# Performance work log

Measured on AMD Instinct MI355X. Metric: run time of the kernel, lower is better.

The kernel has to match this reference:

```python
import jax, jax.numpy as jnp
import numpy as np
import itertools

# hyperparameters (match init_kwargs cfg)
V_SIZE = 32000; D = 768; H = 12; NL = 2
K_BITS = 4; L_TAB = 4; M_COPIES = 2; HID = 3072
DK = D // H; R = 1 << K_BITS; EPS = 1e-6; RMS_EPS = 1e-5

def _protos_T():
    # corners of the {-1,+1}^K hypercube, transposed -> [K, R]
    corners = np.array(list(itertools.product([-1.0, 1.0], repeat=K_BITS)), dtype=np.float32)
    return jnp.asarray(corners.T)

def setup_inputs() -> dict:
    key = jax.random.key(0)
    ks = jax.random.split(key, 14)
    s = 0.02
    return {
        "in_idx": jax.random.randint(ks[0], (1, 1024), 0, V_SIZE),
        "tok_emb": jax.random.normal(ks[1], (V_SIZE, D), jnp.float32) * s,
        "norm1_w": jnp.ones((NL, D), jnp.float32),
        "qw": jax.random.normal(ks[2], (NL, D, D), jnp.float32) * s,
        "kw": jax.random.normal(ks[3], (NL, D, D), jnp.float32) * s,
        "vw": jax.random.normal(ks[4], (NL, D, D), jnp.float32) * s,
        "ow": jax.random.normal(ks[5], (NL, D, D), jnp.float32) * s,
        "ob": jnp.zeros((NL, D), jnp.float32),
        "norm2_w": jnp.ones((NL, D), jnp.float32),
        "ff_w1": jax.random.normal(ks[6], (NL, D, HID), jnp.float32) * s,
        "ff_w2": jax.random.normal(ks[7], (NL, D, HID), jnp.float32) * s,
        "ff_w3": jax.random.normal(ks[8], (NL, HID, D), jnp.float32) * s,
        "final_norm_w": jnp.ones((D,), jnp.float32),
        "out_w": jax.random.normal(ks[9], (D, V_SIZE), jnp.float32) * s,
        "planes_T": jax.random.normal(ks[10], (NL, M_COPIES, DK, L_TAB * K_BITS), jnp.float32),
    }

def _rmsnorm(x, w):
    return x * jax.lax.rsqrt(jnp.mean(x * x, axis=-1, keepdims=True) + RMS_EPS) * w

def _race_attention(h, qw, kw, vw, ow, ob, planes, protos_T):
    B, T, _ = h.shape
    Q = (h @ qw).reshape(B, T, H, DK)
    Kt = (h @ kw).reshape(B, T, H, DK)
    Vt = (h @ vw).reshape(B, T, H, DK)
    # RoPE (split-even/odd, concat halves variant, start position 0)
    theta = 10000.0 ** (-jnp.arange(0, DK, 2, dtype=jnp.float32) / DK)
    freq = jnp.arange(T, dtype=jnp.float32)[:, None] * theta[None, :]  # [T, DK/2]
    sin = jnp.sin(freq)[None, :, None, :]
    cos = jnp.cos(freq)[None, :, None, :]
    def rope(z):
        e, o = z[..., ::2], z[..., 1::2]
        return jnp.concatenate([e * cos - o * sin, e * sin + o * cos], axis=-1)
    Q, Kt = rope(Q), rope(Kt)
    to_hb = lambda z: jnp.transpose(z, (0, 2, 1, 3)).reshape(B * H, T, DK)
    Qh, Kh, Vh = to_hb(Q), to_hb(Kt), to_hb(Vt)
    N = M_COPIES * B * H
    scale = jnp.sqrt(jnp.float32(DK))
    # random-plane projections per model copy m: [M, BH, T, L*K]
    projK = jnp.einsum('ntd,mds->mnts', Kh, planes).reshape(N, T, L_TAB, K_BITS)
    projQ = jnp.einsum('ntd,mds->mnts', Qh, planes).reshape(N, T, L_TAB, K_BITS)
    probsK = jax.nn.softmax((jnp.tanh(projK) / scale) @ protos_T, axis=-1)  # [N,T,L,R]
    probsQ = jax.nn.softmax((jnp.tanh(projQ) / scale) @ protos_T, axis=-1)
    Vn = jnp.broadcast_to(Vh[None], (M_COPIES, B * H, T, DK)).reshape(N, T, DK)
    # causal prefix sums over time
    A_pref = jnp.cumsum(probsK, axis=1)                                     # [N,T,L,R]
    B_pref = jnp.cumsum(probsK[..., None] * Vn[:, :, None, None, :], axis=1)  # [N,T,L,R,DK]
    E_pref = B_pref / (A_pref[..., None] + EPS)
    out2 = jnp.einsum('ntlr,ntlrd->ntd', probsQ, E_pref)                    # [N,T,DK]
    out_h = out2.reshape(M_COPIES, B, H, T, DK).transpose(0, 1, 3, 2, 4)    # [M,B,T,H,DK]
    m = out_h.mean(axis=0)                                                  # [B,T,H,DK]
    # faithful to the source: permute to [B,H,T,DK] then row-major reshape to [B,T,H*DK]
    out = jnp.transpose(m, (0, 2, 1, 3)).reshape(B, T, H * DK)
    return out @ ow + ob

def reference(in_idx, tok_emb, norm1_w, qw, kw, vw, ow, ob, norm2_w,
              ff_w1, ff_w2, ff_w3, final_norm_w, out_w, planes_T):
    protos_T = _protos_T()
    x = tok_emb[in_idx]  # [B,T,D]
    for l in range(NL):
        h = _rmsnorm(x, norm1_w[l])
        x = x + _race_attention(h, qw[l], kw[l], vw[l], ow[l], ob[l], planes_T[l], protos_T)
        h = _rmsnorm(x, norm2_w[l])
        x = x + (jax.nn.silu(h @ ff_w1[l]) * (h @ ff_w2[l])) @ ff_w3[l]
    x = _rmsnorm(x, final_norm_w)
    return x @ out_w  # logits [B,T,V]
```

## Files before the change

kernel.cpp:

```cpp
#include <hip/hip_runtime.h>
#include <hip/hip_bf16.h>

#define T_SEQ 1024
#define D_MODEL 768
#define QKVW 2304
#define NHEAD 12
#define NLAYER 2
#define MCOPY 2
#define HID_DIM 3072
#define VSIZE 32000
#define NCH 32
#define TL 32

typedef __attribute__((ext_vector_type(8))) short short8;
typedef __attribute__((ext_vector_type(4))) float f32x4;

__device__ __forceinline__ short f2bf(float f) {
  unsigned u = __builtin_bit_cast(unsigned, f);
  u = (u + 0x7FFFu + ((u >> 16) & 1u)) >> 16;
  return (short)u;
}

__global__ __launch_bounds__(64) void stc_k(float* __restrict__ stc) {
  int t = blockIdx.x;
  int i = threadIdx.x;
  if (i < 32) {
    float theta = powf(10000.0f, -(float)i / 32.0f);
    float s, c;
    sincosf((float)t * theta, &s, &c);
    stc[t * 64 + 2 * i] = c;
    stc[t * 64 + 2 * i + 1] = s;
  }
}

__global__ __launch_bounds__(256) void embed_norm_k(const int* __restrict__ idx,
                                                    const float* __restrict__ emb,
                                                    const float* __restrict__ w,
                                                    float* __restrict__ x,
                                                    short* __restrict__ out) {
  int t = blockIdx.x, tid = threadIdx.x;
  int r = idx[t];
  float v[3];
  float ss = 0.f;
  #pragma unroll
  for (int j = 0; j < 3; ++j) {
    int i = tid + j * 256;
    float val = emb[(size_t)r * D_MODEL + i];
    x[(size_t)t * D_MODEL + i] = val;
    v[j] = val;
    ss += val * val;
  }
  __shared__ float red[256];
  red[tid] = ss; __syncthreads();
  for (int s = 128; s > 0; s >>= 1) {
    if (tid < s) red[tid] += red[tid + s];
    __syncthreads();
  }
  float inv = rsqrtf(red[0] / (float)D_MODEL + 1e-5f);
  #pragma unroll
  for (int j = 0; j < 3; ++j) {
    int i = tid + j * 256;
    out[(size_t)t * D_MODEL + i] = f2bf(v[j] * inv * w[i]);
  }
}

__global__ __launch_bounds__(256) void add_norm_k(float* __restrict__ x,
                                                  const float* __restrict__ parts,
                                                  int nparts,
                                                  const float* __restrict__ bias,
                                                  const float* __restrict__ w,
                                                  short* __restrict__ out) {
  int t = blockIdx.x, tid = threadIdx.x;
  float v[3];
  float ss = 0.f;
  #pragma unroll
  for (int j = 0; j < 3; ++j) {
    int i = tid + j * 256;
    float val = x[(size_t)t * D_MODEL + i];
    if (bias) val += bias[i];
    for (int p = 0; p < nparts; ++p)
      val += parts[(size_t)p * (T_SEQ * D_MODEL) + (size_t)t * D_MODEL + i];
    v[j] = val;
    ss += val * val;
  }
  __shared__ float red[256];
  red[tid] = ss; __syncthreads();
  for (int s = 128; s > 0; s >>= 1) {
    if (tid < s) red[tid] += red[tid + s];
    __syncthreads();
  }
  float inv = rsqrtf(red[0] / (float)D_MODEL + 1e-5f);
  #pragma unroll
  for (int j = 0; j < 3; ++j) {
    int i = tid + j * 256;
    if (nparts || bias) x[(size_t)t * D_MODEL + i] = v[j];
    out[(size_t)t * D_MODEL + i] = f2bf(v[j] * inv * w[i]);
  }
}

__device__ __forceinline__ void tr_tile(const float* __restrict__ W,
                                        short* __restrict__ WT, int K, int N,
                                        int n0, int k0, int tx, int ty) {
  __shared__ float tile[32][33];
  #pragma unroll
  for (int i = 0; i < 4; ++i)
    tile[ty + 8 * i][tx] = W[(size_t)(k0 + ty + 8 * i) * N + n0 + tx];
  __syncthreads();
  #pragma unroll
  for (int i = 0; i < 4; ++i)
    WT[(size_t)(n0 + ty + 8 * i) * K + k0 + tx] = f2bf(tile[tx][ty + 8 * i]);
}

#define SQ_W  ((size_t)D_MODEL * D_MODEL)
#define FF_W  ((size_t)D_MODEL * HID_DIM)
#define LAYER_W (4 * SQ_W + 3 * FF_W)

__global__ __launch_bounds__(256) void transpose_sq8(const float* __restrict__ qw,
                                                     const float* __restrict__ kw,
                                                     const float* __restrict__ vw,
                                                     const float* __restrict__ ow,
                                                     short* __restrict__ WB) {
  int z = blockIdx.z, layer = z >> 2, which = z & 3;
  const float* W = (which == 0) ? qw : (which == 1) ? kw : (which == 2) ? vw : ow;
  W += (size_t)layer * SQ_W;
  short* WT = WB + (size_t)layer * LAYER_W + (size_t)which * SQ_W;
  tr_tile(W, WT, D_MODEL, D_MODEL, blockIdx.x * 32, blockIdx.y * 32,
          threadIdx.x, threadIdx.y);
}

__global__ __launch_bounds__(256) void transpose_ff12(const float* __restrict__ W1g,
                                                      const float* __restrict__ W2g,
                                                      short* __restrict__ WB) {
  __shared__ float tile[32][33];
  int layer = blockIdx.z;
  const float* W1 = W1g + (size_t)layer * FF_W;
  const float* W2 = W2g + (size_t)layer * FF_W;
  short* WT = WB + (size_t)layer * LAYER_W + 4 * SQ_W;
  int tx = threadIdx.x, ty = threadIdx.y;
  int n0 = blockIdx.x * 32, k0 = blockIdx.y * 32;
  int h0 = n0 >> 1;
  const float* src = (tx < 16) ? (W1 + h0 + tx) : (W2 + h0 + (tx - 16));
  #pragma unroll
  for (int i = 0; i < 4; ++i)
    tile[ty + 8 * i][tx] = src[(size_t)(k0 + ty + 8 * i) * HID_DIM];
  __syncthreads();
  #pragma unroll
  for (int i = 0; i < 4; ++i) {
    int n = ty + 8 * i;
    WT[(size_t)(n0 + n) * D_MODEL + k0 + tx] = f2bf(tile[tx][n]);
  }
}

__global__ __launch_bounds__(256) void transpose_f3(const float* __restrict__ W3g,
                                                    short* __restrict__ WB) {
  int layer = blockIdx.z;
  const float* W = W3g + (size_t)layer * FF_W;
  short* WT = WB + (size_t)layer * LAYER_W + 4 * SQ_W + 2 * FF_W;
  tr_tile(W, WT, HID_DIM, D_MODEL, blockIdx.x * 32, blockIdx.y * 32,
          threadIdx.x, threadIdx.y);
}

__global__ __launch_bounds__(256) void transpose_head(const float* __restrict__ W,
                                                      short* __restrict__ WT) {
  tr_tile(W, WT, D_MODEL, VSIZE, blockIdx.x * 32, blockIdx.y * 32,
          threadIdx.x, threadIdx.y);
}

template<int NROW32>
__device__ __forceinline__ void stage_rows(const short* __restrict__ gbase,
                                           int ldK, short* lds, int tid) {
  #pragma unroll
  for (int j = 0; j < NROW32; ++j) {
    int r = j * 32 + (tid >> 3);
    int s = tid & 7;
    const short* gp = gbase + (size_t)r * ldK + (((s ^ (r & 7))) << 3);
    short* lp = lds + j * 2048 + tid * 8;
    __builtin_amdgcn_global_load_lds((const __attribute__((address_space(1))) void*)gp,
                                     (__attribute__((address_space(3))) void*)lp,
                                     16, 0, 0);
  }
}

__device__ __forceinline__ short8 frag_ld(const short* lds, int row, int sl) {
  return *(const short8*)(lds + row * 64 + ((sl ^ (row & 7)) << 3));
}

template<int MODE, int DBUF>
__global__ __launch_bounds__(256) void gemm_t(const short* __restrict__ A,
                                              const short* __restrict__ Bt,
                                              float* __restrict__ Cf,
                                              short* __restrict__ Cs,
                                              int N, int K) {
  __shared__ short As[DBUF + 1][128 * 64];
  __shared__ short Bs[DBUF + 1][128 * 64];
  int tid = threadIdx.x;
  int lane = tid & 63;
  int wave = tid >> 6;
  int wr = wave >> 1, wc = wave & 1;
  int l15 = lane & 15, kg = lane >> 4;

  int cpx = gridDim.x >> 3;
  int wg = (blockIdx.x & 7) * cpx + (blockIdx.x >> 3);
  int row0 = (wg & 7) * 128;
  int col0 = (wg >> 3) * 128;

  int kn = K / gridDim.y;
  int koff = blockIdx.y * kn;
  const short* Ab = A + (size_t)row0 * K + koff;
  const short* Bb = Bt + (size_t)col0 * K + koff;
  int nt = kn >> 6;

  f32x4 acc[4][4] = {};

  if constexpr (DBUF) {
    stage_rows<4>(Ab, K, As[0], tid);
    stage_rows<4>(Bb, K, Bs[0], tid);
    __syncthreads();
  }

  int cur = 0;
  for (int t = 0; t < nt; ++t) {
    if constexpr (DBUF) {
      if (t + 1 < nt) {
        stage_rows<4>(Ab + (t + 1) * 64, K, As[cur ^ 1], tid);
        stage_rows<4>(Bb + (t + 1) * 64, K, Bs[cur ^ 1], tid);
      }
    } else {
      stage_rows<4>(Ab + t * 64, K, As[0], tid);
      stage_rows<4>(Bb + t * 64, K, Bs[0], tid);
      __syncthreads();
    }
    const short* Ac = As[cur];
    const short* Bc = Bs[cur];
    #pragma unroll
    for (int kk = 0; kk < 2; ++kk) {
      short8 af[4], bf4[4];
      #pragma unroll
      for (int m = 0; m < 4; ++m)
        af[m] = frag_ld(Ac, wr * 64 + m * 16 + l15, 4 * kk + kg);
      #pragma unroll
      for (int n = 0; n < 4; ++n)
        bf4[n] = frag_ld(Bc, wc * 64 + n * 16 + l15, 4 * kk + kg);
      #pragma unroll
      for (int m = 0; m < 4; ++m)
        #pragma unroll
        for (int n = 0; n < 4; ++n)
          acc[m][n] = __builtin_amdgcn_mfma_f32_16x16x32_bf16(af[m], bf4[n], acc[m][n], 0, 0, 0);
    }
    __syncthreads();
    if constexpr (DBUF) cur ^= 1;
  }

  int rbase = (lane >> 4) * 4;
  if constexpr (MODE == 2) {
    int base = col0 + wc * 64;
    #pragma unroll
    for (int p = 0; p < 2; ++p) {
      int h = (base >> 1) + p * 16 + l15;
      #pragma unroll
      for (int m = 0; m < 4; ++m) {
        #pragma unroll
        for (int r = 0; r < 4; ++r) {
          int row = row0 + wr * 64 + m * 16 + rbase + r;
          float g1 = acc[m][2 * p][r];
          float g2 = acc[m][2 * p + 1][r];
          Cs[(size_t)row * HID_DIM + h] = f2bf((g1 / (1.f + expf(-g1))) * g2);
        }
      }
    }
  } else {
    float* Co = Cf;
    if constexpr (MODE == 1) Co += (size_t)blockIdx.y * T_SEQ * N;
    #pragma unroll
    for (int n = 0; n < 4; ++n) {
      int col = col0 + wc * 64 + n * 16 + l15;
      #pragma unroll
      for (int m = 0; m < 4; ++m) {
        #pragma unroll
        for (int r = 0; r < 4; ++r) {
          int row = row0 + wr * 64 + m * 16 + rbase + r;
          Co[(size_t)row * N + col] = acc[m][n][r];
        }
      }
    }
  }
}

template<int MODE>
__global__ __launch_bounds__(256) void gemm64(const short* __restrict__ A,
                                              const short* __restrict__ Bt,
                                              float* __restrict__ Cf,
                                              int N, int K) {
  __shared__ short As[2][64 * 64];
  __shared__ short Bs[2][128 * 64];
  int tid = threadIdx.x;
  int lane = tid & 63;
  int wave = tid >> 6;
  int l15 = lane & 15, kg = lane >> 4;

  int cpx = gridDim.x >> 3;
  int wg = (blockIdx.x & 7) * cpx + (blockIdx.x >> 3);
  int row0 = (wg & 15) * 64;
  int col0 = (wg >> 4) * 128;

  int kn = K / gridDim.y;
  int koff = blockIdx.y * kn;
  const short* Ab = A + (size_t)row0 * K + koff;
  const short* Bb = Bt + (size_t)col0 * K + koff;
  int nt = kn >> 6;

  f32x4 acc[4][2] = {};

  stage_rows<2>(Ab, K, As[0], tid);
  stage_rows<4>(Bb, K, Bs[0], tid);
  __syncthreads();

  int cur = 0;
  for (int t = 0; t < nt; ++t) {
    if (t + 1 < nt) {
      stage_rows<2>(Ab + (t + 1) * 64, K, As[cur ^ 1], tid);
      stage_rows<4>(Bb + (t + 1) * 64, K, Bs[cur ^ 1], tid);
    }
    const short* Ac = As[cur];
    const short* Bc = Bs[cur];
    #pragma unroll
    for (int kk = 0; kk < 2; ++kk) {
      short8 af[4], bf2[2];
      #pragma unroll
      for (int m = 0; m < 4; ++m)
        af[m] = frag_ld(Ac, m * 16 + l15, 4 * kk + kg);
      #pragma unroll
      for (int n = 0; n < 2; ++n)
        bf2[n] = frag_ld(Bc, wave * 32 + n * 16 + l15, 4 * kk + kg);
      #pragma unroll
      for (int m = 0; m < 4; ++m)
        #pragma unroll
        for (int n = 0; n < 2; ++n)
          acc[m][n] = __builtin_amdgcn_mfma_f32_16x16x32_bf16(af[m], bf2[n], acc[m][n], 0, 0, 0);
    }
    __syncthreads();
    cur ^= 1;
  }

  int rbase = (lane >> 4) * 4;
  float* Co = Cf;
  if constexpr (MODE == 1) Co += (size_t)blockIdx.y * T_SEQ * N;
  #pragma unroll
  for (int n = 0; n < 2; ++n) {
    int col = col0 + wave * 32 + n * 16 + l15;
    #pragma unroll
    for (int m = 0; m < 4; ++m) {
      #pragma unroll
      for (int r = 0; r < 4; ++r) {
        int row = row0 + m * 16 + rbase + r;
        Co[(size_t)row * N + col] = acc[m][n][r];
      }
    }
  }
}

__global__ __launch_bounds__(256) void race_probs(const float* __restrict__ qkv,
                                                  const float* __restrict__ stc,
                                                  const float* __restrict__ planes,
                                                  float* __restrict__ pq,
                                                  float* __restrict__ pk) {
  int gid = blockIdx.x * 256 + threadIdx.x;
  int w = gid & 1;
  int l = (gid >> 1) & 3;
  int t = (gid >> 3) & 1023;
  int mn = gid >> 13;
  int m = mn / NHEAD, n = mn % NHEAD;
  const float* raw = qkv + (size_t)t * QKVW + (w ? 0 : D_MODEL) + n * 64;
  const float* sc = stc + t * 64;
  const float* pl = planes + m * 64 * 16 + l * 4;
  float p0 = 0.f, p1 = 0.f, p2 = 0.f, p3 = 0.f;
  #pragma unroll 4
  for (int i = 0; i < 32; ++i) {
    float e = raw[2 * i], o = raw[2 * i + 1];
    float c = sc[2 * i], s = sc[2 * i + 1];
    float re = e * c - o * s;
    float ro = e * s + o * c;
    const float* pe = pl + i * 16;
    const float* po = pl + (i + 32) * 16;
    p0 += re * pe[0] + ro * po[0];
    p1 += re * pe[1] + ro * po[1];
    p2 += re * pe[2] + ro * po[2];
    p3 += re * pe[3] + ro * po[3];
  }
  float t0 = tanhf(p0) * 0.125f;
  float t1 = tanhf(p1) * 0.125f;
  float t2 = tanhf(p2) * 0.125f;
  float t3 = tanhf(p3) * 0.125f;
  float lg[16];
  float mx = -1e30f;
  #pragma unroll
  for (int r = 0; r < 16; ++r) {
    float s = ((r & 8) ? t0 : -t0) + ((r & 4) ? t1 : -t1) +
              ((r & 2) ? t2 : -t2) + ((r & 1) ? t3 : -t3);
    lg[r] = s;
    mx = fmaxf(mx, s);
  }
  float sum = 0.f;
  #pragma unroll
  for (int r = 0; r < 16; ++r) {
    float e = expf(lg[r] - mx);
    lg[r] = e;
    sum += e;
  }
  float inv = 1.f / sum;
  float* dst = (w ? pq : pk) + ((size_t)mn * T_SEQ + t) * 64 + l * 16;
  #pragma unroll
  for (int r = 0; r < 16; ++r) dst[r] = lg[r] * inv;
}

__global__ __launch_bounds__(256) void race_chunksum(const float* __restrict__ pk_g,
                                                     const float* __restrict__ v_g,
                                                     float* __restrict__ csA,
                                                     float* __restrict__ csB) {
  int mn = blockIdx.x, ch = blockIdx.y;
  int n = mn % NHEAD;
  int tid = threadIdx.x;
  int wave = tid >> 6, lane = tid & 63;
  int l15 = lane & 15, g = lane >> 4;
  int d = wave * 16 + l15;
  __shared__ float L[2][2][64];
  const float* pkrow = pk_g + ((size_t)mn * T_SEQ + (size_t)ch * TL) * 64;
  const float* vrow = v_g + (size_t)(ch * TL) * QKVW + n * 64;

  float a[16], bp[16];
  #pragma unroll
  for (int i = 0; i < 16; ++i) { a[i] = 0.f; bp[i] = 0.f; }

  float r0 = 0.f;
  if (wave == 0) r0 = pkrow[lane];
  else if (wave == 1) r0 = vrow[lane];

  int cur = 0;
  #pragma unroll 1
  for (int t = 0; t < TL; ++t) {
    if (wave < 2) L[cur][wave][lane] = r0;
    __syncthreads();
    if (t + 1 < TL) {
      if (wave == 0) r0 = pkrow[(t + 1) * 64 + lane];
      else if (wave == 1) r0 = vrow[(size_t)(t + 1) * QKVW + lane];
    }
    float vd = L[cur][1][d];
    #pragma unroll
    for (int i = 0; i < 16; ++i) {
      float p = L[cur][0][g * 16 + i];
      a[i] += p;
      bp[i] = fmaf(p, vd, bp[i]);
    }
    cur ^= 1;
  }
  size_t base = ((size_t)mn * NCH + ch) * 64;
  if (wave == 0 && l15 == 0) {
    #pragma unroll
    for (int i = 0; i < 16; ++i) csA[base + g * 16 + i] = a[i];
  }
  #pragma unroll
  for (int i = 0; i < 16; ++i) csB[(base + g * 16 + i) * 64 + d] = bp[i];
}

__global__ __launch_bounds__(64) void race_chunkscan(float* __restrict__ csA,
                                                     float* __restrict__ csB) {
  int mn = blockIdx.x, lr = blockIdx.y;
  int d = threadIdx.x;
  float runB = 0.f, runA = 0.f;
  for (int c = 0; c < NCH; ++c) {
    size_t ib = (((size_t)mn * NCH + c) * 64 + lr) * 64 + d;
    float b = csB[ib];
    csB[ib] = runB;
    runB += b;
    if (d == 0) {
      size_t ia = ((size_t)mn * NCH + c) * 64 + lr;
      float av = csA[ia];
      csA[ia] = runA;
      runA += av;
    }
  }
}

__global__ __launch_bounds__(256) void race_scan_emit(const float* __restrict__ pk_g,
                                                      const float* __restrict__ pq_g,
                                                      const float* __restrict__ v_g,
                                                      const float* __restrict__ csA,
                                                      const float* __restrict__ csB,
                                                      short* __restrict__ ro) {
  int n = blockIdx.x, ch = blockIdx.y;
  int tid = threadIdx.x;
  int wave = tid >> 6, lane = tid & 63;
  int l15 = lane & 15, g = lane >> 4;
  int d = wave * 16 + l15;
  int mn0 = n, mn1 = NHEAD + n;
  __shared__ float L[2][5][64];

  const float* pk0r = pk_g + ((size_t)mn0 * T_SEQ + (size_t)ch * TL) * 64;
  const float* pk1r = pk_g + ((size_t)mn1 * T_SEQ + (size_t)ch * TL) * 64;
  const float* pq0r = pq_g + ((size_t)mn0 * T_SEQ + (size_t)ch * TL) * 64;
  const float* pq1r = pq_g + ((size_t)mn1 * T_SEQ + (size_t)ch * TL) * 64;
  const float* vrow = v_g + (size_t)(ch * TL) * QKVW + n * 64;
  const float* src0 = (wave == 0) ? pk0r : (wave == 1) ? pk1r
                    : (wave == 2) ? pq0r : pq1r;

  float a0[16], b0[16], a1[16], b1[16];
  size_t base0 = ((size_t)mn0 * NCH + ch) * 64;
  size_t base1 = ((size_t)mn1 * NCH + ch) * 64;
  #pragma unroll
  for (int i = 0; i < 16; ++i) {
    a0[i] = csA[base0 + g * 16 + i];
    b0[i] = csB[(base0 + g * 16 + i) * 64 + d];
    a1[i] = csA[base1 + g * 16 + i];
    b1[i] = csB[(base1 + g * 16 + i) * 64 + d];
  }

  float r0 = src0[lane];
  float r1 = (wave == 0) ? vrow[lane] : 0.f;

  int cur = 0;
  #pragma unroll 1
  for (int t = 0; t < TL; ++t) {
    L[cur][wave][lane] = r0;
    if (wave == 0) L[cur][4][lane] = r1;
    __syncthreads();
    if (t + 1 < TL) {
      r0 = src0[(t + 1) * 64 + lane];
      if (wave == 0) r1 = vrow[(size_t)(t + 1) * QKVW + lane];
    }
    float vd = L[cur][4][d];
    float c = 0.f;
    #pragma unroll
    for (int i = 0; i < 16; ++i) {
      int lr = g * 16 + i;
      float p = L[cur][0][lr];
      a0[i] += p;
      b0[i] = fmaf(p, vd, b0[i]);
      c = fmaf(L[cur][2][lr] * b0[i], __builtin_amdgcn_rcpf(a0[i] + 1e-6f), c);
      p = L[cur][1][lr];
      a1[i] += p;
      b1[i] = fmaf(p, vd, b1[i]);
      c = fmaf(L[cur][3][lr] * b1[i], __builtin_amdgcn_rcpf(a1[i] + 1e-6f), c);
    }
    c += __shfl_xor(c, 16);
    c += __shfl_xor(c, 32);
    if (g == 0)
      ro[n * (T_SEQ * 64) + (ch * TL + t) * 64 + d] = f2bf(0.5f * c);
    cur ^= 1;
  }
}

extern "C" void kernel_launch(void* const* d_in, const int* in_sizes, int n_in,
                              void* d_out, int out_size, void* d_ws, size_t ws_size,
                              hipStream_t stream) {
  const int*   in_idx       = (const int*)d_in[0];
  const float* tok_emb      = (const float*)d_in[1];
  const float* norm1_w      = (const float*)d_in[2];
  const float* qw           = (const float*)d_in[3];
  const float* kw           = (const float*)d_in[4];
  const float* vw           = (const float*)d_in[5];
  const float* ow           = (const float*)d_in[6];
  const float* ob           = (const float*)d_in[7];
  const float* norm2_w      = (const float*)d_in[8];
  const float* ff_w1        = (const float*)d_in[9];
  const float* ff_w2        = (const float*)d_in[10];
  const float* ff_w3        = (const float*)d_in[11];
  const float* final_norm_w = (const float*)d_in[12];
  const float* out_w        = (const float*)d_in[13];
  const float* planes       = (const float*)d_in[14];

  float* ws = (float*)d_ws;
  const size_t SZ_TD = (size_t)T_SEQ * D_MODEL;
  float* X   = ws;
  float* STC = X + SZ_TD;
  float* S   = STC + 65536;
  short* HbB = (short*)S;
  float* QKV = S + 393216;
  float* PK  = QKV + (size_t)T_SEQ * QKVW;
  float* PQ  = PK + (size_t)MCOPY * NHEAD * T_SEQ * 64;
  float* CSA = PQ + (size_t)MCOPY * NHEAD * T_SEQ * 64;
  float* CSB = CSA + (size_t)MCOPY * NHEAD * NCH * 64;
  short* ROb = (short*)(CSB + (size_t)MCOPY * NHEAD * NCH * 64 * 64);
  short* G1B = (short*)QKV;
  float* PP  = PK;
  short* WB = (short*)(S + 9486336);
  short* outT = WB + NLAYER * LAYER_W;

  stc_k<<<T_SEQ, 64, 0, stream>>>(STC);
  dim3 tb(32, 8);
  transpose_sq8<<<dim3(24, 24, 8), tb, 0, stream>>>(qw, kw, vw, ow, WB);
  transpose_ff12<<<dim3(192, 24, 2), tb, 0, stream>>>(ff_w1, ff_w2, WB);
  transpose_f3<<<dim3(24, 96, 2), tb, 0, stream>>>(ff_w3, WB);
  transpose_head<<<dim3(1000, 24), tb, 0, stream>>>(out_w, outT);

  embed_norm_k<<<T_SEQ, 256, 0, stream>>>(in_idx, tok_emb, norm1_w, X, HbB);

  for (int l = 0; l < NLAYER; ++l) {
    short* base = WB + (size_t)l * LAYER_W;
    short* qkvT = base;
    short* owT  = base + 3 * SQ_W;
    short* f12T = base + 4 * SQ_W;
    short* f3T  = base + 4 * SQ_W + 2 * FF_W;

    gemm64<0><<<dim3(16 * (QKVW / 128), 1), 256, 0, stream>>>(HbB, qkvT, QKV, QKVW, D_MODEL);
    race_probs<<<(MCOPY * NHEAD * T_SEQ * 4 * 2) / 256, 256, 0, stream>>>(
        QKV, STC, planes + (size_t)l * MCOPY * 64 * 16, PQ, PK);
    dim3 gps(MCOPY * NHEAD, NCH);
    race_chunksum<<<gps, 256, 0, stream>>>(PK, QKV + 2 * D_MODEL, CSA, CSB);
    dim3 gcs(MCOPY * NHEAD, 64);
    race_chunkscan<<<gcs, 64, 0, stream>>>(CSA, CSB);
    dim3 gemit(NHEAD, NCH);
    race_scan_emit<<<gemit, 256, 0, stream>>>(PK, PQ, QKV + 2 * D_MODEL, CSA, CSB, ROb);
    gemm64<1><<<dim3(16 * (D_MODEL / 128), 2), 256, 0, stream>>>(ROb, owT, PP, D_MODEL, D_MODEL);
    add_norm_k<<<T_SEQ, 256, 0, stream>>>(X, PP, 2, ob + l * D_MODEL, norm2_w + l * D_MODEL, HbB);
    gemm_t<2, 1><<<dim3(8 * (2 * HID_DIM / 128), 1), 256, 0, stream>>>(HbB, f12T, nullptr, G1B, 2 * HID_DIM, D_MODEL);
    gemm64<1><<<dim3(16 * (D_MODEL / 128), 4), 256, 0, stream>>>(G1B, f3T, PP, D_MODEL, HID_DIM);
    const float* nw = (l == NLAYER - 1) ? final_norm_w : norm1_w + (l + 1) * D_MODEL;
    add_norm_k<<<T_SEQ, 256, 0, stream>>>(X, PP, 4, nullptr, nw, HbB);
  }
  gemm_t<0, 0><<<dim3(8 * (VSIZE / 128), 1), 256, 0, stream>>>(HbB, outT, (float*)d_out, nullptr, VSIZE, D_MODEL);
}
```

Measured before the change: 466.3 us.

## Use 64-row tiles for FF gate GEMM and raise split-K on output projections

The FF1/FF2 gate GEMM moves from the 128-row gemm_t kernel to gemm64 with a new MODE 2 epilogue. That epilogue applies SiLU-gating to paired columns (the weights are assumed interleaved per 16-column group) and writes bf16 directly. Split-K doubles for the attention output projection (2→4) and the FF3 projection (4→8), with add_norm reducing more partials. The race_probs loop also switches to float2/float4 vectorized loads. Together these aim to raise occupancy and parallelism on these small-M GEMMs, at the cost of extra partial-sum traffic.

```diff
diff --git a/kernel.cpp b/kernel.cpp
--- a/kernel.cpp
+++ b/kernel.cpp
@@ -290,6 +290,7 @@
 __global__ __launch_bounds__(256) void gemm64(const short* __restrict__ A,
                                               const short* __restrict__ Bt,
                                               float* __restrict__ Cf,
+                                              short* __restrict__ Cs,
                                               int N, int K) {
   __shared__ short As[2][64 * 64];
   __shared__ short Bs[2][128 * 64];
@@ -343,17 +344,32 @@
   }
 
   int rbase = (lane >> 4) * 4;
-  float* Co = Cf;
-  if constexpr (MODE == 1) Co += (size_t)blockIdx.y * T_SEQ * N;
-  #pragma unroll
-  for (int n = 0; n < 2; ++n) {
-    int col = col0 + wave * 32 + n * 16 + l15;
+  if constexpr (MODE == 2) {
+    int c0 = col0 + wave * 32;
+    int h = (c0 >> 1) + l15;
     #pragma unroll
     for (int m = 0; m < 4; ++m) {
       #pragma unroll
       for (int r = 0; r < 4; ++r) {
         int row = row0 + m * 16 + rbase + r;
-        Co[(size_t)row * N + col] = acc[m][n][r];
+        float g1 = acc[m][0][r];
+        float g2 = acc[m][1][r];
+        Cs[(size_t)row * HID_DIM + h] = f2bf((g1 / (1.f + expf(-g1))) * g2);
+      }
+    }
+  } else {
+    float* Co = Cf;
+    if constexpr (MODE == 1) Co += (size_t)blockIdx.y * T_SEQ * N;
+    #pragma unroll
+    for (int n = 0; n < 2; ++n) {
+      int col = col0 + wave * 32 + n * 16 + l15;
+      #pragma unroll
+      for (int m = 0; m < 4; ++m) {
+        #pragma unroll
+        for (int r = 0; r < 4; ++r) {
+          int row = row0 + m * 16 + rbase + r;
+          Co[(size_t)row * N + col] = acc[m][n][r];
+        }
       }
     }
   }
@@ -376,16 +392,16 @@
   float p0 = 0.f, p1 = 0.f, p2 = 0.f, p3 = 0.f;
   #pragma unroll 4
   for (int i = 0; i < 32; ++i) {
-    float e = raw[2 * i], o = raw[2 * i + 1];
-    float c = sc[2 * i], s = sc[2 * i + 1];
-    float re = e * c - o * s;
-    float ro = e * s + o * c;
-    const float* pe = pl + i * 16;
-    const float* po = pl + (i + 32) * 16;
-    p0 += re * pe[0] + ro * po[0];
-    p1 += re * pe[1] + ro * po[1];
-    p2 += re * pe[2] + ro * po[2];
-    p3 += re * pe[3] + ro * po[3];
+    float2 eo = ((const float2*)raw)[i];
+    float2 cs = ((const float2*)sc)[i];
+    float re = eo.x * cs.x - eo.y * cs.y;
+    float ro = eo.x * cs.y + eo.y * cs.x;
+    float4 pe = *(const float4*)(pl + i * 16);
+    float4 po = *(const float4*)(pl + (i + 32) * 16);
+    p0 += re * pe.x + ro * po.x;
+    p1 += re * pe.y + ro * po.y;
+    p2 += re * pe.z + ro * po.z;
+    p3 += re * pe.w + ro * po.w;
   }
   float t0 = tanhf(p0) * 0.125f;
   float t1 = tanhf(p1) * 0.125f;
@@ -601,7 +617,7 @@
     short* f12T = base + 4 * SQ_W;
     short* f3T  = base + 4 * SQ_W + 2 * FF_W;
 
-    gemm64<0><<<dim3(16 * (QKVW / 128), 1), 256, 0, stream>>>(HbB, qkvT, QKV, QKVW, D_MODEL);
+    gemm64<0><<<dim3(16 * (QKVW / 128), 1), 256, 0, stream>>>(HbB, qkvT, QKV, nullptr, QKVW, D_MODEL);
     race_probs<<<(MCOPY * NHEAD * T_SEQ * 4 * 2) / 256, 256, 0, stream>>>(
         QKV, STC, planes + (size_t)l * MCOPY * 64 * 16, PQ, PK);
     dim3 gps(MCOPY * NHEAD, NCH);
@@ -610,12 +626,12 @@
     race_chunkscan<<<gcs, 64, 0, stream>>>(CSA, CSB);
     dim3 gemit(NHEAD, NCH);
     race_scan_emit<<<gemit, 256, 0, stream>>>(PK, PQ, QKV + 2 * D_MODEL, CSA, CSB, ROb);
-    gemm64<1><<<dim3(16 * (D_MODEL / 128), 2), 256, 0, stream>>>(ROb, owT, PP, D_MODEL, D_MODEL);
-    add_norm_k<<<T_SEQ, 256, 0, stream>>>(X, PP, 2, ob + l * D_MODEL, norm2_w + l * D_MODEL, HbB);
-    gemm_t<2, 1><<<dim3(8 * (2 * HID_DIM / 128), 1), 256, 0, stream>>>(HbB, f12T, nullptr, G1B, 2 * HID_DIM, D_MODEL);
-    gemm64<1><<<dim3(16 * (D_MODEL / 128), 4), 256, 0, stream>>>(G1B, f3T, PP, D_MODEL, HID_DIM);
+    gemm64<1><<<dim3(16 * (D_MODEL / 128), 4), 256, 0, stream>>>(ROb, owT, PP, nullptr, D_MODEL, D_MODEL);
+    add_norm_k<<<T_SEQ, 256, 0, stream>>>(X, PP, 4, ob + l * D_MODEL, norm2_w + l * D_MODEL, HbB);
+    gemm64<2><<<dim3(16 * (2 * HID_DIM / 128), 1), 256, 0, stream>>>(HbB, f12T, nullptr, G1B, 2 * HID_DIM, D_MODEL);
+    gemm64<1><<<dim3(16 * (D_MODEL / 128), 8), 256, 0, stream>>>(G1B, f3T, PP, nullptr, D_MODEL, HID_DIM);
     const float* nw = (l == NLAYER - 1) ? final_norm_w : norm1_w + (l + 1) * D_MODEL;
-    add_norm_k<<<T_SEQ, 256, 0, stream>>>(X, PP, 4, nullptr, nw, HbB);
+    add_norm_k<<<T_SEQ, 256, 0, stream>>>(X, PP, 8, nullptr, nw, HbB);
   }
   gemm_t<0, 0><<<dim3(8 * (VSIZE / 128), 1), 256, 0, stream>>>(HbB, outT, (float*)d_out, nullptr, VSIZE, D_MODEL);
 }
```

Measured after the change: 469.2 us. No clear change (+0.6%).
